# Optimization experiments

Measured on AMD Instinct MI355X. Metric: run time of the kernel, lower is better.

The kernel has to match this reference:

```python
import jax, jax.numpy as jnp
import numpy as np

GAMMA = 0.99
GAE_LAMBDA = 0.95
CLIP_PARAM = 0.2
VALUE_LOSS_COEF = 0.5
ENTROPY_COEF = 0.01
T, N = 1024, 8192

def setup_inputs() -> dict:
    key = jax.random.key(0)
    ks = jax.random.split(key, 9)
    rewards = jax.random.normal(ks[0], (T, N, 1), dtype=jnp.float32)
    masks = (jax.random.uniform(ks[1], (T + 1, N, 1)) > 0.02).astype(jnp.float32)
    bad_masks = (jax.random.uniform(ks[2], (T + 1, N, 1)) > 0.01).astype(jnp.float32)
    value_preds = jax.random.normal(ks[3], (T + 1, N, 1), dtype=jnp.float32)
    last_value = jax.random.normal(ks[4], (N, 1), dtype=jnp.float32)
    log_prob = jax.random.normal(ks[5], (T, N, 1), dtype=jnp.float32) * 0.1
    prev_log_prob = jax.random.normal(ks[6], (T, N, 1), dtype=jnp.float32) * 0.1
    new_value = jax.random.normal(ks[7], (T, N, 1), dtype=jnp.float32)
    dist_entropy = jax.random.normal(ks[8], (T, N, 1), dtype=jnp.float32)
    return {"rewards": rewards, "masks": masks, "bad_masks": bad_masks,
            "value_preds": value_preds, "last_value": last_value,
            "log_prob": log_prob, "prev_log_prob": prev_log_prob,
            "new_value": new_value, "dist_entropy": dist_entropy}


def _compute_derived(rewards, masks, bad_masks, value_preds, last_value):
    # value_preds is detached in the original update(); mirror with stop_gradient
    vp = jax.lax.stop_gradient(value_preds)
    lv = jax.lax.stop_gradient(last_value)
    vp = vp.at[-1].set(lv)  # value_preds[-1] = last_value

    def step(gae, xs):
        r, v_next, v, m_next, bad_next = xs
        delta = r + GAMMA * v_next * m_next - v
        gae = (delta + GAMMA * GAE_LAMBDA * m_next * gae) * bad_next
        return gae, gae + v  # returns[step] = gae + value_preds[step]

    xs = (rewards, vp[1:], vp[:-1], masks[1:], bad_masks[1:])
    init = jnp.zeros_like(lv)
    _, returns_t = jax.lax.scan(step, init, xs, reverse=True)  # (T, N, 1)

    advantages = returns_t - vp[:-1]
    advantages = (advantages - advantages.mean()) / (advantages.std(ddof=1) + 1e-5)
    return advantages, returns_t


def reference(rewards, masks, bad_masks, value_preds, last_value,
              log_prob, prev_log_prob, new_value, dist_entropy):
    advantages, returns_t = _compute_derived(rewards, masks, bad_masks,
                                             value_preds, last_value)
    # PPO clipped surrogate (single minibatch = full rollout, flattened over T*N)
    ratio = jnp.exp(log_prob - prev_log_prob)
    surr1 = ratio * advantages
    surr2 = jnp.clip(ratio, 1.0 - CLIP_PARAM, 1.0 + CLIP_PARAM) * advantages
    action_loss = -jnp.minimum(surr1, surr2).mean()

    value_target = jax.lax.stop_gradient(returns_t)
    old_value = jax.lax.stop_gradient(value_preds[:-1])
    value_pred_clipped = old_value + jnp.clip(new_value - old_value,
                                              -CLIP_PARAM, CLIP_PARAM)
    value_losses = (new_value - value_target) ** 2
    value_losses_clipped = (value_pred_clipped - value_target) ** 2
    value_loss = 0.5 * jnp.maximum(value_losses, value_losses_clipped).mean()

    loss = (value_loss * VALUE_LOSS_COEF + action_loss
            - dist_entropy.mean() * ENTROPY_COEF)
    return loss
```

## Files before the change

kernel.cpp:

```cpp
#include <hip/hip_runtime.h>
#include <math.h>

#define T_DIM 1024
#define N_DIM 8192
#define M_TOT (T_DIM * N_DIM)
#define NVEC  (M_TOT / 4)
#define NV4   (N_DIM / 4)
#define L_CHUNK 8
#define C_CHUNKS 128

#define PC_BLOCKS   ((C_CHUNKS * NV4) / 256)
#define LOSS_BLOCKS 2048
#define LOSS_STRIDE (LOSS_BLOCKS * 256)

#define kGAMMA 0.99f
#define kGLAM  (0.99f * 0.95f)


__device__ __forceinline__ unsigned short f2bf(float f) {
    unsigned int u = __float_as_uint(f);
    u += 0x7fffu + ((u >> 16) & 1u);
    return (unsigned short)(u >> 16);
}
__device__ __forceinline__ float bf2f(unsigned short h) {
    return __uint_as_float(((unsigned int)h) << 16);
}

__global__ __launch_bounds__(256) void k_pc(
    const float4* __restrict__ r4,
    const float4* __restrict__ m4,
    const float4* __restrict__ bm4,
    const float4* __restrict__ vp4,
    const float4* __restrict__ lv4,
    ushort4* __restrict__ b16,
    float4* __restrict__ A_out,
    float4* __restrict__ B_out)
{
    const int g  = blockIdx.x * 256 + threadIdx.x;
    const int j  = g & (NV4 - 1);
    const int c  = g >> 11;
    const int t0 = c * L_CHUNK;

    float4 vnext = (c == C_CHUNKS - 1) ? lv4[j] : vp4[(t0 + L_CHUNK) * NV4 + j];
    float4 Aa = make_float4(1.f, 1.f, 1.f, 1.f);
    float4 Bb = make_float4(0.f, 0.f, 0.f, 0.f);

    #pragma unroll
    for (int i = L_CHUNK - 1; i >= 0; --i) {
        const int idx = (t0 + i) * NV4 + j;
        const float4 r  = r4[idx];
        const float4 v  = vp4[idx];
        const float4 m  = m4[idx + NV4];
        const float4 bb = bm4[idx + NV4];

        ushort4 o;
        {
            const float b = (fmaf(kGAMMA * m.x, vnext.x, r.x) - v.x) * bb.x;
            const float a = kGLAM * m.x * bb.x;
            Aa.x = a * Aa.x; Bb.x = fmaf(a, Bb.x, b);
            o.x = (unsigned short)((f2bf(b) & 0xFFFEu) | ((m.x * bb.x > 0.5f) ? 1u : 0u));
        }
        {
            const float b = (fmaf(kGAMMA * m.y, vnext.y, r.y) - v.y) * bb.y;
            const float a = kGLAM * m.y * bb.y;
            Aa.y = a * Aa.y; Bb.y = fmaf(a, Bb.y, b);
            o.y = (unsigned short)((f2bf(b) & 0xFFFEu) | ((m.y * bb.y > 0.5f) ? 1u : 0u));
        }
        {
            const float b = (fmaf(kGAMMA * m.z, vnext.z, r.z) - v.z) * bb.z;
            const float a = kGLAM * m.z * bb.z;
            Aa.z = a * Aa.z; Bb.z = fmaf(a, Bb.z, b);
            o.z = (unsigned short)((f2bf(b) & 0xFFFEu) | ((m.z * bb.z > 0.5f) ? 1u : 0u));
        }
        {
            const float b = (fmaf(kGAMMA * m.w, vnext.w, r.w) - v.w) * bb.w;
            const float a = kGLAM * m.w * bb.w;
            Aa.w = a * Aa.w; Bb.w = fmaf(a, Bb.w, b);
            o.w = (unsigned short)((f2bf(b) & 0xFFFEu) | ((m.w * bb.w > 0.5f) ? 1u : 0u));
        }
        b16[idx] = o;
        vnext = v;
    }
    A_out[c * NV4 + j] = Aa;
    B_out[c * NV4 + j] = Bb;
}

__global__ __launch_bounds__(256) void k_ginc(
    const float* __restrict__ A_in,
    const float* __restrict__ B_in,
    float* __restrict__ g_in)
{
    const int n = blockIdx.x * 256 + threadIdx.x;
    float g = 0.0f;
    constexpr int PB = 16;
    for (int cb = C_CHUNKS - PB; cb >= 0; cb -= PB) {
        float Ar[PB], Br[PB];
        #pragma unroll
        for (int i = 0; i < PB; ++i) {
            Ar[i] = A_in[(cb + i) * N_DIM + n];
            Br[i] = B_in[(cb + i) * N_DIM + n];
        }
        #pragma unroll
        for (int i = PB - 1; i >= 0; --i) {
            g_in[(cb + i) * N_DIM + n] = g;
            g = fmaf(Ar[i], g, Br[i]);
        }
    }
}

__device__ __forceinline__ void gae_comp(float& gae, unsigned short h,
                                         float v, float nvv,
                                         float& sg, float& sg2, float& v_s) {
    const float bf = bf2f(h);
    const float a  = (h & 1u) ? kGLAM : 0.0f;
    gae = fmaf(a, gae, bf);
    sg += gae;
    sg2 = fmaf(gae, gae, sg2);
    const float q  = nvv - v;
    const float e1 = q - gae;
    const float e2 = fminf(fmaxf(q, -0.2f), 0.2f) - gae;
    v_s += fmaxf(e1 * e1, e2 * e2);
}

__global__ __launch_bounds__(256) void k_gae(
    ushort4* __restrict__ bg16,
    const float4* __restrict__ g_in4,
    const float4* __restrict__ vp4,
    const float4* __restrict__ nv4,
    double* __restrict__ pg)
{
    const int g  = blockIdx.x * 256 + threadIdx.x;
    const int j  = g & (NV4 - 1);
    const int c  = g >> 11;
    const int t0 = c * L_CHUNK;

    float4 gae = g_in4[c * NV4 + j];
    float sg = 0.f, sg2 = 0.f, v_s = 0.f;

    #pragma unroll
    for (int i = L_CHUNK - 1; i >= 0; --i) {
        const int idx = (t0 + i) * NV4 + j;
        const ushort4 h = bg16[idx];
        const float4  v = vp4[idx];
        const float4  q = nv4[idx];
        gae_comp(gae.x, h.x, v.x, q.x, sg, sg2, v_s);
        gae_comp(gae.y, h.y, v.y, q.y, sg, sg2, v_s);
        gae_comp(gae.z, h.z, v.z, q.z, sg, sg2, v_s);
        gae_comp(gae.w, h.w, v.w, q.w, sg, sg2, v_s);
        ushort4 o;
        o.x = f2bf(gae.x); o.y = f2bf(gae.y); o.z = f2bf(gae.z); o.w = f2bf(gae.w);
        bg16[idx] = o;
    }

    double d0 = (double)sg, d1 = (double)sg2, d2 = (double)v_s;
    #pragma unroll
    for (int off = 32; off > 0; off >>= 1) {
        d0 += __shfl_down(d0, off, 64);
        d1 += __shfl_down(d1, off, 64);
        d2 += __shfl_down(d2, off, 64);
    }
    __shared__ double sh[3][4];
    const int wid = threadIdx.x >> 6, lane = threadIdx.x & 63;
    if (lane == 0) { sh[0][wid] = d0; sh[1][wid] = d1; sh[2][wid] = d2; }
    __syncthreads();
    if (threadIdx.x == 0) {
        double t0s = 0, t1s = 0, t2s = 0;
        #pragma unroll
        for (int w = 0; w < 4; ++w) { t0s += sh[0][w]; t1s += sh[1][w]; t2s += sh[2][w]; }
        pg[blockIdx.x * 3 + 0] = t0s;
        pg[blockIdx.x * 3 + 1] = t1s;
        pg[blockIdx.x * 3 + 2] = t2s;
    }
}

__global__ __launch_bounds__(256) void k_stats(
    const double* __restrict__ pg, double* __restrict__ acc)
{
    double s0 = 0.0, s1 = 0.0, s2 = 0.0;
    for (int i = threadIdx.x; i < PC_BLOCKS; i += 256) {
        s0 += pg[i * 3 + 0];
        s1 += pg[i * 3 + 1];
        s2 += pg[i * 3 + 2];
    }
    #pragma unroll
    for (int off = 32; off > 0; off >>= 1) {
        s0 += __shfl_down(s0, off, 64);
        s1 += __shfl_down(s1, off, 64);
        s2 += __shfl_down(s2, off, 64);
    }
    __shared__ double sh[3][4];
    const int wid = threadIdx.x >> 6, lane = threadIdx.x & 63;
    if (lane == 0) { sh[0][wid] = s0; sh[1][wid] = s1; sh[2][wid] = s2; }
    __syncthreads();
    if (threadIdx.x == 0) {
        double sum = 0, sum2 = 0, vsum = 0;
        #pragma unroll
        for (int w = 0; w < 4; ++w) { sum += sh[0][w]; sum2 += sh[1][w]; vsum += sh[2][w]; }
        const double M = (double)M_TOT;
        const double mu = sum / M;
        double var = (sum2 - sum * sum / M) / (M - 1.0);
        if (var < 0.0) var = 0.0;
        acc[3] = vsum;
        acc[5] = mu;
        acc[6] = 1.0 / (sqrt(var) + 1e-5);
    }
}

__global__ __launch_bounds__(256) void k_loss(
    const ushort4* __restrict__ gae16,
    const float4* __restrict__ lp4,
    const float4* __restrict__ plp4,
    const float4* __restrict__ ent4,
    const double* __restrict__ acc,
    double* __restrict__ pl)
{
    const int tid = blockIdx.x * 256 + threadIdx.x;
    const float mu   = (float)acc[5];
    const float invs = (float)acc[6];

    float a_s = 0.f, e_s = 0.f;
    #pragma unroll
    for (int k = 0; k < 4; ++k) {
        const int i = tid + k * LOSS_STRIDE;
        const ushort4 G = gae16[i];
        const float4  L = lp4[i];
        const float4  P = plp4[i];
        const float4  E = ent4[i];
        const float gs[4] = {bf2f(G.x), bf2f(G.y), bf2f(G.z), bf2f(G.w)};
        const float ls[4] = {L.x, L.y, L.z, L.w};
        const float ps[4] = {P.x, P.y, P.z, P.w};
        #pragma unroll
        for (int c = 0; c < 4; ++c) {
            const float x  = (gs[c] - mu) * invs;
            const float r  = __expf(ls[c] - ps[c]);
            const float rc = fminf(fmaxf(r, 0.8f), 1.2f);
            a_s += fminf(r * x, rc * x);
        }
        e_s += E.x + E.y + E.z + E.w;
    }

    double d0 = (double)a_s, d1 = (double)e_s;
    #pragma unroll
    for (int off = 32; off > 0; off >>= 1) {
        d0 += __shfl_down(d0, off, 64);
        d1 += __shfl_down(d1, off, 64);
    }
    __shared__ double sh[2][4];
    const int wid = threadIdx.x >> 6, lane = threadIdx.x & 63;
    if (lane == 0) { sh[0][wid] = d0; sh[1][wid] = d1; }
    __syncthreads();
    if (threadIdx.x == 0) {
        double t0s = 0, t1s = 0;
        #pragma unroll
        for (int w = 0; w < 4; ++w) { t0s += sh[0][w]; t1s += sh[1][w]; }
        pl[blockIdx.x * 2 + 0] = t0s;
        pl[blockIdx.x * 2 + 1] = t1s;
    }
}

__global__ __launch_bounds__(256) void k_final(
    const double* __restrict__ pl, const double* __restrict__ acc,
    float* __restrict__ out)
{
    double s0 = 0.0, s1 = 0.0;
    for (int i = threadIdx.x; i < LOSS_BLOCKS; i += 256) {
        s0 += pl[i * 2 + 0];
        s1 += pl[i * 2 + 1];
    }
    #pragma unroll
    for (int off = 32; off > 0; off >>= 1) {
        s0 += __shfl_down(s0, off, 64);
        s1 += __shfl_down(s1, off, 64);
    }
    __shared__ double sh[2][4];
    const int wid = threadIdx.x >> 6, lane = threadIdx.x & 63;
    if (lane == 0) { sh[0][wid] = s0; sh[1][wid] = s1; }
    __syncthreads();
    if (threadIdx.x == 0) {
        double a_sum = 0, e_sum = 0;
        #pragma unroll
        for (int w = 0; w < 4; ++w) { a_sum += sh[0][w]; e_sum += sh[1][w]; }
        const double M = (double)M_TOT;
        out[0] = (float)(0.25 * acc[3] / M - a_sum / M - 0.01 * e_sum / M);
    }
}

extern "C" void kernel_launch(void* const* d_in, const int* in_sizes, int n_in,
                              void* d_out, int out_size, void* d_ws, size_t ws_size,
                              hipStream_t stream) {
    const float* rewards     = (const float*)d_in[0];
    const float* masks       = (const float*)d_in[1];
    const float* bad_masks   = (const float*)d_in[2];
    const float* value_preds = (const float*)d_in[3];
    const float* last_value  = (const float*)d_in[4];
    const float* log_prob    = (const float*)d_in[5];
    const float* prev_lp     = (const float*)d_in[6];
    const float* new_value   = (const float*)d_in[7];
    const float* dist_ent    = (const float*)d_in[8];

    char* ws = (char*)d_ws;
    double* acc = (double*)ws;
    double* pg  = (double*)(ws + 256);
    double* pl  = (double*)(ws + 32768);
    unsigned short* b16 = (unsigned short*)(ws + 65536);
    float* A = (float*)(ws + 65536 + (size_t)M_TOT * 2);
    float* B = (float*)(ws + 65536 + (size_t)M_TOT * 2 + (size_t)C_CHUNKS * N_DIM * 4);

    k_pc<<<PC_BLOCKS, 256, 0, stream>>>((const float4*)rewards,
                                        (const float4*)masks,
                                        (const float4*)bad_masks,
                                        (const float4*)value_preds,
                                        (const float4*)last_value,
                                        (ushort4*)b16, (float4*)A, (float4*)B);
    k_ginc<<<N_DIM / 256, 256, 0, stream>>>(A, B, A );
    k_gae<<<PC_BLOCKS, 256, 0, stream>>>((ushort4*)b16,
                                         (const float4*)A ,
                                         (const float4*)value_preds,
                                         (const float4*)new_value, pg);
    k_stats<<<1, 256, 0, stream>>>(pg, acc);
    k_loss<<<LOSS_BLOCKS, 256, 0, stream>>>((const ushort4*)b16 ,
                                            (const float4*)log_prob,
                                            (const float4*)prev_lp,
                                            (const float4*)dist_ent, acc, pl);
    k_final<<<1, 256, 0, stream>>>(pl, acc, (float*)d_out);
}
```

Before: 274.1 us.

## Run full sequential GAE scan in mid kernel and fuse recompute with loss pass

The chunk-carry (A,B) computation is replaced by a per-column sequential scan over all T steps of the bf16-packed deltas, which also produces the mean/variance sums and the per-chunk carry-in values. The old gae pass (which wrote gae back as bf16) and the separate loss pass are merged into one kernel that recomputes gae from the carries and accumulates action, value and entropy sums in a single sweep. This drops one full read and write of the bf16 buffer and the A/B arrays. In exchange, the mid kernel uses only 32 blocks doing strided 2-byte loads over 1024 steps, which gives little parallelism and may be latency bound.

```diff
diff --git a/kernel.cpp b/kernel.cpp
--- a/kernel.cpp
+++ b/kernel.cpp
@@ -9,9 +9,8 @@
 #define L_CHUNK 8
 #define C_CHUNKS 128
 
-#define PC_BLOCKS   ((C_CHUNKS * NV4) / 256)
-#define LOSS_BLOCKS 2048
-#define LOSS_STRIDE (LOSS_BLOCKS * 256)
+#define PC_BLOCKS  ((C_CHUNKS * NV4) / 256)
+#define MID_BLOCKS (N_DIM / 256)
 
 #define kGAMMA 0.99f
 #define kGLAM  (0.99f * 0.95f)
@@ -32,9 +31,7 @@
     const float4* __restrict__ bm4,
     const float4* __restrict__ vp4,
     const float4* __restrict__ lv4,
-    ushort4* __restrict__ b16,
-    float4* __restrict__ A_out,
-    float4* __restrict__ B_out)
+    ushort4* __restrict__ b16)
 {
     const int g  = blockIdx.x * 256 + threadIdx.x;
     const int j  = g & (NV4 - 1);
@@ -42,8 +39,6 @@
     const int t0 = c * L_CHUNK;
 
     float4 vnext = (c == C_CHUNKS - 1) ? lv4[j] : vp4[(t0 + L_CHUNK) * NV4 + j];
-    float4 Aa = make_float4(1.f, 1.f, 1.f, 1.f);
-    float4 Bb = make_float4(0.f, 0.f, 0.f, 0.f);
 
     #pragma unroll
     for (int i = L_CHUNK - 1; i >= 0; --i) {
@@ -56,232 +51,197 @@
         ushort4 o;
         {
             const float b = (fmaf(kGAMMA * m.x, vnext.x, r.x) - v.x) * bb.x;
-            const float a = kGLAM * m.x * bb.x;
-            Aa.x = a * Aa.x; Bb.x = fmaf(a, Bb.x, b);
             o.x = (unsigned short)((f2bf(b) & 0xFFFEu) | ((m.x * bb.x > 0.5f) ? 1u : 0u));
         }
         {
             const float b = (fmaf(kGAMMA * m.y, vnext.y, r.y) - v.y) * bb.y;
-            const float a = kGLAM * m.y * bb.y;
-            Aa.y = a * Aa.y; Bb.y = fmaf(a, Bb.y, b);
             o.y = (unsigned short)((f2bf(b) & 0xFFFEu) | ((m.y * bb.y > 0.5f) ? 1u : 0u));
         }
         {
             const float b = (fmaf(kGAMMA * m.z, vnext.z, r.z) - v.z) * bb.z;
-            const float a = kGLAM * m.z * bb.z;
-            Aa.z = a * Aa.z; Bb.z = fmaf(a, Bb.z, b);
             o.z = (unsigned short)((f2bf(b) & 0xFFFEu) | ((m.z * bb.z > 0.5f) ? 1u : 0u));
         }
         {
             const float b = (fmaf(kGAMMA * m.w, vnext.w, r.w) - v.w) * bb.w;
-            const float a = kGLAM * m.w * bb.w;
-            Aa.w = a * Aa.w; Bb.w = fmaf(a, Bb.w, b);
             o.w = (unsigned short)((f2bf(b) & 0xFFFEu) | ((m.w * bb.w > 0.5f) ? 1u : 0u));
         }
         b16[idx] = o;
         vnext = v;
     }
-    A_out[c * NV4 + j] = Aa;
-    B_out[c * NV4 + j] = Bb;
-}
-
-__global__ __launch_bounds__(256) void k_ginc(
-    const float* __restrict__ A_in,
-    const float* __restrict__ B_in,
-    float* __restrict__ g_in)
+}
+
+__global__ __launch_bounds__(256) void k_mid(
+    const unsigned short* __restrict__ b16,
+    float* __restrict__ g_in,
+    double* __restrict__ pm)
 {
     const int n = blockIdx.x * 256 + threadIdx.x;
-    float g = 0.0f;
-    constexpr int PB = 16;
-    for (int cb = C_CHUNKS - PB; cb >= 0; cb -= PB) {
-        float Ar[PB], Br[PB];
-        #pragma unroll
-        for (int i = 0; i < PB; ++i) {
-            Ar[i] = A_in[(cb + i) * N_DIM + n];
-            Br[i] = B_in[(cb + i) * N_DIM + n];
-        }
+    float g = 0.f, sg = 0.f, sg2 = 0.f;
+
+    constexpr int PB = 32;
+    for (int tb = T_DIM - PB; tb >= 0; tb -= PB) {
+        unsigned short h[PB];
+        #pragma unroll
+        for (int i = 0; i < PB; ++i) h[i] = b16[(tb + i) * N_DIM + n];
         #pragma unroll
         for (int i = PB - 1; i >= 0; --i) {
-            g_in[(cb + i) * N_DIM + n] = g;
-            g = fmaf(Ar[i], g, Br[i]);
-        }
-    }
-}
-
-__device__ __forceinline__ void gae_comp(float& gae, unsigned short h,
-                                         float v, float nvv,
-                                         float& sg, float& sg2, float& v_s) {
-    const float bf = bf2f(h);
-    const float a  = (h & 1u) ? kGLAM : 0.0f;
-    gae = fmaf(a, gae, bf);
-    sg += gae;
-    sg2 = fmaf(gae, gae, sg2);
-    const float q  = nvv - v;
-    const float e1 = q - gae;
-    const float e2 = fminf(fmaxf(q, -0.2f), 0.2f) - gae;
-    v_s += fmaxf(e1 * e1, e2 * e2);
-}
-
-__global__ __launch_bounds__(256) void k_gae(
-    ushort4* __restrict__ bg16,
+            const int t = tb + i;
+            if ((t & (L_CHUNK - 1)) == (L_CHUNK - 1)) {
+                g_in[(t >> 3) * N_DIM + n] = g;
+            }
+            const float bf = bf2f(h[i]);
+            const float a  = (h[i] & 1u) ? kGLAM : 0.0f;
+            g = fmaf(a, g, bf);
+            sg += g;
+            sg2 = fmaf(g, g, sg2);
+        }
+    }
+
+    double d0 = (double)sg, d1 = (double)sg2;
+    #pragma unroll
+    for (int off = 32; off > 0; off >>= 1) {
+        d0 += __shfl_down(d0, off, 64);
+        d1 += __shfl_down(d1, off, 64);
+    }
+    __shared__ double sh[2][4];
+    const int wid = threadIdx.x >> 6, lane = threadIdx.x & 63;
+    if (lane == 0) { sh[0][wid] = d0; sh[1][wid] = d1; }
+    __syncthreads();
+    if (threadIdx.x == 0) {
+        double t0s = 0, t1s = 0;
+        #pragma unroll
+        for (int w = 0; w < 4; ++w) { t0s += sh[0][w]; t1s += sh[1][w]; }
+        pm[blockIdx.x * 2 + 0] = t0s;
+        pm[blockIdx.x * 2 + 1] = t1s;
+    }
+}
+
+__global__ __launch_bounds__(64) void k_stats(
+    const double* __restrict__ pm, double* __restrict__ acc)
+{
+    double s0 = 0.0, s1 = 0.0;
+    if (threadIdx.x < MID_BLOCKS) {
+        s0 = pm[threadIdx.x * 2 + 0];
+        s1 = pm[threadIdx.x * 2 + 1];
+    }
+    #pragma unroll
+    for (int off = 32; off > 0; off >>= 1) {
+        s0 += __shfl_down(s0, off, 64);
+        s1 += __shfl_down(s1, off, 64);
+    }
+    if (threadIdx.x == 0) {
+        const double M = (double)M_TOT;
+        const double mu = s0 / M;
+        double var = (s1 - s0 * s0 / M) / (M - 1.0);
+        if (var < 0.0) var = 0.0;
+        acc[0] = mu;
+        acc[1] = 1.0 / (sqrt(var) + 1e-5);
+    }
+}
+
+__global__ __launch_bounds__(256) void k_big(
+    const ushort4* __restrict__ b16,
     const float4* __restrict__ g_in4,
     const float4* __restrict__ vp4,
     const float4* __restrict__ nv4,
-    double* __restrict__ pg)
-{
-    const int g  = blockIdx.x * 256 + threadIdx.x;
-    const int j  = g & (NV4 - 1);
-    const int c  = g >> 11;
-    const int t0 = c * L_CHUNK;
-
-    float4 gae = g_in4[c * NV4 + j];
-    float sg = 0.f, sg2 = 0.f, v_s = 0.f;
-
-    #pragma unroll
-    for (int i = L_CHUNK - 1; i >= 0; --i) {
-        const int idx = (t0 + i) * NV4 + j;
-        const ushort4 h = bg16[idx];
-        const float4  v = vp4[idx];
-        const float4  q = nv4[idx];
-        gae_comp(gae.x, h.x, v.x, q.x, sg, sg2, v_s);
-        gae_comp(gae.y, h.y, v.y, q.y, sg, sg2, v_s);
-        gae_comp(gae.z, h.z, v.z, q.z, sg, sg2, v_s);
-        gae_comp(gae.w, h.w, v.w, q.w, sg, sg2, v_s);
-        ushort4 o;
-        o.x = f2bf(gae.x); o.y = f2bf(gae.y); o.z = f2bf(gae.z); o.w = f2bf(gae.w);
-        bg16[idx] = o;
-    }
-
-    double d0 = (double)sg, d1 = (double)sg2, d2 = (double)v_s;
-    #pragma unroll
-    for (int off = 32; off > 0; off >>= 1) {
-        d0 += __shfl_down(d0, off, 64);
-        d1 += __shfl_down(d1, off, 64);
-        d2 += __shfl_down(d2, off, 64);
-    }
-    __shared__ double sh[3][4];
-    const int wid = threadIdx.x >> 6, lane = threadIdx.x & 63;
-    if (lane == 0) { sh[0][wid] = d0; sh[1][wid] = d1; sh[2][wid] = d2; }
-    __syncthreads();
-    if (threadIdx.x == 0) {
-        double t0s = 0, t1s = 0, t2s = 0;
-        #pragma unroll
-        for (int w = 0; w < 4; ++w) { t0s += sh[0][w]; t1s += sh[1][w]; t2s += sh[2][w]; }
-        pg[blockIdx.x * 3 + 0] = t0s;
-        pg[blockIdx.x * 3 + 1] = t1s;
-        pg[blockIdx.x * 3 + 2] = t2s;
-    }
-}
-
-__global__ __launch_bounds__(256) void k_stats(
-    const double* __restrict__ pg, double* __restrict__ acc)
-{
-    double s0 = 0.0, s1 = 0.0, s2 = 0.0;
-    for (int i = threadIdx.x; i < PC_BLOCKS; i += 256) {
-        s0 += pg[i * 3 + 0];
-        s1 += pg[i * 3 + 1];
-        s2 += pg[i * 3 + 2];
-    }
-    #pragma unroll
-    for (int off = 32; off > 0; off >>= 1) {
-        s0 += __shfl_down(s0, off, 64);
-        s1 += __shfl_down(s1, off, 64);
-        s2 += __shfl_down(s2, off, 64);
-    }
-    __shared__ double sh[3][4];
-    const int wid = threadIdx.x >> 6, lane = threadIdx.x & 63;
-    if (lane == 0) { sh[0][wid] = s0; sh[1][wid] = s1; sh[2][wid] = s2; }
-    __syncthreads();
-    if (threadIdx.x == 0) {
-        double sum = 0, sum2 = 0, vsum = 0;
-        #pragma unroll
-        for (int w = 0; w < 4; ++w) { sum += sh[0][w]; sum2 += sh[1][w]; vsum += sh[2][w]; }
-        const double M = (double)M_TOT;
-        const double mu = sum / M;
-        double var = (sum2 - sum * sum / M) / (M - 1.0);
-        if (var < 0.0) var = 0.0;
-        acc[3] = vsum;
-        acc[5] = mu;
-        acc[6] = 1.0 / (sqrt(var) + 1e-5);
-    }
-}
-
-__global__ __launch_bounds__(256) void k_loss(
-    const ushort4* __restrict__ gae16,
     const float4* __restrict__ lp4,
     const float4* __restrict__ plp4,
     const float4* __restrict__ ent4,
     const double* __restrict__ acc,
     double* __restrict__ pl)
 {
-    const int tid = blockIdx.x * 256 + threadIdx.x;
-    const float mu   = (float)acc[5];
-    const float invs = (float)acc[6];
-
-    float a_s = 0.f, e_s = 0.f;
-    #pragma unroll
-    for (int k = 0; k < 4; ++k) {
-        const int i = tid + k * LOSS_STRIDE;
-        const ushort4 G = gae16[i];
-        const float4  L = lp4[i];
-        const float4  P = plp4[i];
-        const float4  E = ent4[i];
-        const float gs[4] = {bf2f(G.x), bf2f(G.y), bf2f(G.z), bf2f(G.w)};
+    const int g  = blockIdx.x * 256 + threadIdx.x;
+    const int j  = g & (NV4 - 1);
+    const int c  = g >> 11;
+    const int t0 = c * L_CHUNK;
+
+    const float mu   = (float)acc[0];
+    const float invs = (float)acc[1];
+
+    float4 gae = g_in4[c * NV4 + j];
+    float a_s = 0.f, v_s = 0.f, e_s = 0.f;
+
+    #pragma unroll
+    for (int i = L_CHUNK - 1; i >= 0; --i) {
+        const int idx = (t0 + i) * NV4 + j;
+        const ushort4 h = b16[idx];
+        const float4  v = vp4[idx];
+        const float4  q = nv4[idx];
+        const float4  L = lp4[idx];
+        const float4  P = plp4[idx];
+        const float4  E = ent4[idx];
+
+        const unsigned short hh[4] = {h.x, h.y, h.z, h.w};
+        const float vs[4] = {v.x, v.y, v.z, v.w};
+        const float qs[4] = {q.x, q.y, q.z, q.w};
         const float ls[4] = {L.x, L.y, L.z, L.w};
         const float ps[4] = {P.x, P.y, P.z, P.w};
-        #pragma unroll
-        for (int c = 0; c < 4; ++c) {
-            const float x  = (gs[c] - mu) * invs;
-            const float r  = __expf(ls[c] - ps[c]);
+        float gg[4] = {gae.x, gae.y, gae.z, gae.w};
+
+        #pragma unroll
+        for (int u = 0; u < 4; ++u) {
+            const float bf = bf2f(hh[u]);
+            const float a  = (hh[u] & 1u) ? kGLAM : 0.0f;
+            gg[u] = fmaf(a, gg[u], bf);
+            const float d  = qs[u] - vs[u];
+            const float e1 = d - gg[u];
+            const float e2 = fminf(fmaxf(d, -0.2f), 0.2f) - gg[u];
+            v_s += fmaxf(e1 * e1, e2 * e2);
+            const float x  = (gg[u] - mu) * invs;
+            const float r  = __expf(ls[u] - ps[u]);
             const float rc = fminf(fmaxf(r, 0.8f), 1.2f);
             a_s += fminf(r * x, rc * x);
         }
         e_s += E.x + E.y + E.z + E.w;
-    }
-
-    double d0 = (double)a_s, d1 = (double)e_s;
+        gae.x = gg[0]; gae.y = gg[1]; gae.z = gg[2]; gae.w = gg[3];
+    }
+
+    double d0 = (double)a_s, d1 = (double)v_s, d2 = (double)e_s;
     #pragma unroll
     for (int off = 32; off > 0; off >>= 1) {
         d0 += __shfl_down(d0, off, 64);
         d1 += __shfl_down(d1, off, 64);
-    }
-    __shared__ double sh[2][4];
+        d2 += __shfl_down(d2, off, 64);
+    }
+    __shared__ double sh[3][4];
     const int wid = threadIdx.x >> 6, lane = threadIdx.x & 63;
-    if (lane == 0) { sh[0][wid] = d0; sh[1][wid] = d1; }
+    if (lane == 0) { sh[0][wid] = d0; sh[1][wid] = d1; sh[2][wid] = d2; }
     __syncthreads();
     if (threadIdx.x == 0) {
-        double t0s = 0, t1s = 0;
-        #pragma unroll
-        for (int w = 0; w < 4; ++w) { t0s += sh[0][w]; t1s += sh[1][w]; }
-        pl[blockIdx.x * 2 + 0] = t0s;
-        pl[blockIdx.x * 2 + 1] = t1s;
+        double t0s = 0, t1s = 0, t2s = 0;
+        #pragma unroll
+        for (int w = 0; w < 4; ++w) { t0s += sh[0][w]; t1s += sh[1][w]; t2s += sh[2][w]; }
+        pl[blockIdx.x * 3 + 0] = t0s;
+        pl[blockIdx.x * 3 + 1] = t1s;
+        pl[blockIdx.x * 3 + 2] = t2s;
     }
 }
 
 __global__ __launch_bounds__(256) void k_final(
-    const double* __restrict__ pl, const double* __restrict__ acc,
-    float* __restrict__ out)
-{
-    double s0 = 0.0, s1 = 0.0;
-    for (int i = threadIdx.x; i < LOSS_BLOCKS; i += 256) {
-        s0 += pl[i * 2 + 0];
-        s1 += pl[i * 2 + 1];
+    const double* __restrict__ pl, float* __restrict__ out)
+{
+    double s0 = 0.0, s1 = 0.0, s2 = 0.0;
+    for (int i = threadIdx.x; i < PC_BLOCKS; i += 256) {
+        s0 += pl[i * 3 + 0];
+        s1 += pl[i * 3 + 1];
+        s2 += pl[i * 3 + 2];
     }
     #pragma unroll
     for (int off = 32; off > 0; off >>= 1) {
         s0 += __shfl_down(s0, off, 64);
         s1 += __shfl_down(s1, off, 64);
-    }
-    __shared__ double sh[2][4];
+        s2 += __shfl_down(s2, off, 64);
+    }
+    __shared__ double sh[3][4];
     const int wid = threadIdx.x >> 6, lane = threadIdx.x & 63;
-    if (lane == 0) { sh[0][wid] = s0; sh[1][wid] = s1; }
+    if (lane == 0) { sh[0][wid] = s0; sh[1][wid] = s1; sh[2][wid] = s2; }
     __syncthreads();
     if (threadIdx.x == 0) {
-        double a_sum = 0, e_sum = 0;
-        #pragma unroll
-        for (int w = 0; w < 4; ++w) { a_sum += sh[0][w]; e_sum += sh[1][w]; }
+        double a_sum = 0, v_sum = 0, e_sum = 0;
+        #pragma unroll
+        for (int w = 0; w < 4; ++w) { a_sum += sh[0][w]; v_sum += sh[1][w]; e_sum += sh[2][w]; }
         const double M = (double)M_TOT;
-        out[0] = (float)(0.25 * acc[3] / M - a_sum / M - 0.01 * e_sum / M);
+        out[0] = (float)(0.25 * v_sum / M - a_sum / M - 0.01 * e_sum / M);
     }
 }
 
@@ -300,27 +260,26 @@
 
     char* ws = (char*)d_ws;
     double* acc = (double*)ws;
-    double* pg  = (double*)(ws + 256);
-    double* pl  = (double*)(ws + 32768);
+    double* pm  = (double*)(ws + 256);
+    double* pl  = (double*)(ws + 1024);
     unsigned short* b16 = (unsigned short*)(ws + 65536);
-    float* A = (float*)(ws + 65536 + (size_t)M_TOT * 2);
-    float* B = (float*)(ws + 65536 + (size_t)M_TOT * 2 + (size_t)C_CHUNKS * N_DIM * 4);
+    float* g_in = (float*)(ws + 65536 + (size_t)M_TOT * 2);
 
     k_pc<<<PC_BLOCKS, 256, 0, stream>>>((const float4*)rewards,
                                         (const float4*)masks,
                                         (const float4*)bad_masks,
                                         (const float4*)value_preds,
                                         (const float4*)last_value,
-                                        (ushort4*)b16, (float4*)A, (float4*)B);
-    k_ginc<<<N_DIM / 256, 256, 0, stream>>>(A, B, A );
-    k_gae<<<PC_BLOCKS, 256, 0, stream>>>((ushort4*)b16,
-                                         (const float4*)A ,
+                                        (ushort4*)b16);
+    k_mid<<<MID_BLOCKS, 256, 0, stream>>>(b16, g_in, pm);
+    k_stats<<<1, 64, 0, stream>>>(pm, acc);
+    k_big<<<PC_BLOCKS, 256, 0, stream>>>((const ushort4*)b16,
+                                         (const float4*)g_in,
                                          (const float4*)value_preds,
-                                         (const float4*)new_value, pg);
-    k_stats<<<1, 256, 0, stream>>>(pg, acc);
-    k_loss<<<LOSS_BLOCKS, 256, 0, stream>>>((const ushort4*)b16 ,
-                                            (const float4*)log_prob,
-                                            (const float4*)prev_lp,
-                                            (const float4*)dist_ent, acc, pl);
-    k_final<<<1, 256, 0, stream>>>(pl, acc, (float*)d_out);
-}
+                                         (const float4*)new_value,
+                                         (const float4*)log_prob,
+                                         (const float4*)prev_lp,
+                                         (const float4*)dist_ent,
+                                         acc, pl);
+    k_final<<<1, 256, 0, stream>>>(pl, (float*)d_out);
+}
```

Measured after the change: 289.4 us. +5.6%, slower.
